# Performance work log

Measured on AMD Instinct MI355X. Metric: run time of the kernel, lower is better.

## Reference

```python
import jax, jax.numpy as jnp
import numpy as np

B, N, C, H = 64, 577, 768, 12
D = C // H
SCALE = D ** -0.5


def setup_inputs() -> dict:
    key = jax.random.key(0)
    ks = jax.random.split(key, 5)
    s = 0.02
    return {
        "x": jax.random.normal(ks[0], (B, N, C), dtype=jnp.float32),
        "qkv_w": jax.random.normal(ks[1], (3 * C, C), dtype=jnp.float32) * s,
        "qkv_b": jax.random.normal(ks[2], (3 * C,), dtype=jnp.float32) * s,
        "proj_w": jax.random.normal(ks[3], (C, C), dtype=jnp.float32) * s,
        "proj_b": jax.random.normal(ks[4], (C,), dtype=jnp.float32) * s,
    }


def reference(x, qkv_w, qkv_b, proj_w, proj_b):
    b, n, c = x.shape
    # Full QKV projection (as in the original module): [B,N,3C] -> [B,N,3,H,D]
    qkv = (x @ qkv_w.T + qkv_b).reshape(b, n, 3, H, D)
    qc = qkv[:, :1, 0]   # class-token query only: [B,1,H,D]
    k = qkv[:, :, 1]     # [B,N,H,D]
    v = qkv[:, :, 2]     # [B,N,H,D]
    # single-query attention scores per head: [B,H,N]
    attn = jnp.einsum("bohd,bnhd->bhn", qc, k) * SCALE
    attn = jax.nn.softmax(attn, axis=-1)
    # weighted sum of values -> [B,H,D] -> [B,1,C]
    cls = jnp.einsum("bhn,bnhd->bhd", attn, v).reshape(b, 1, c)
    cls = cls @ proj_w.T + proj_b
    return jnp.concatenate([cls, x[:, 1:]], axis=1)
```

## Files before the change

### kernel.cpp

```cpp
#include <hip/hip_runtime.h>

#define Bz 64
#define Nn 577
#define Cc 768
#define Hh 12
#define Dd 64
#define SCALE 0.125f

typedef __attribute__((ext_vector_type(8))) short short8;
typedef __attribute__((ext_vector_type(4))) float float4v;

__device__ __forceinline__ unsigned short bf16rne(float f) {
  unsigned u = __float_as_uint(f);
  u += 0x7FFFu + ((u >> 16) & 1u);
  return (unsigned short)(u >> 16);
}

__device__ __forceinline__ short8 cvt8(float4 a, float4 b) {
  short8 v;
  v[0] = (short)bf16rne(a.x); v[1] = (short)bf16rne(a.y);
  v[2] = (short)bf16rne(a.z); v[3] = (short)bf16rne(a.w);
  v[4] = (short)bf16rne(b.x); v[5] = (short)bf16rne(b.y);
  v[6] = (short)bf16rne(b.z); v[7] = (short)bf16rne(b.w);
  return v;
}


template <int MODE>
__global__ __launch_bounds__(256) void k_gemm64(const float* __restrict__ A,
                                                const float* __restrict__ W,
                                                const float* __restrict__ bias,
                                                float* __restrict__ out) {
  int tile = blockIdx.x;
  int jt = tile % 48, bt = tile / 48;
  int wave = threadIdx.x >> 6, lane = threadIdx.x & 63;
  int m = lane & 15, quad = lane >> 4;
  int brow = bt * 16 + m;
  int jrow = jt * 16 + m;
  size_t aoff;
  if (MODE == 0)      aoff = (size_t)brow * (Nn * Cc);
  else if (MODE == 1) aoff = (size_t)brow * (Hh * Cc) + (size_t)(jt >> 2) * Cc;
  else                aoff = (size_t)brow * Cc;
  size_t woff = (MODE == 1) ? (size_t)(2 * Cc + jrow) * Cc : (size_t)jrow * Cc;
  const float4* Ap = (const float4*)(A + aoff) + wave * 48 + quad * 2;
  const float4* Wp = (const float4*)(W + woff) + wave * 48 + quad * 2;
  float4v acc = {0.f, 0.f, 0.f, 0.f};
#pragma unroll
  for (int s = 0; s < 6; ++s) {
    float4 a0 = Ap[s * 8], a1 = Ap[s * 8 + 1];
    float4 w0 = Wp[s * 8], w1 = Wp[s * 8 + 1];
    acc = __builtin_amdgcn_mfma_f32_16x16x32_bf16(cvt8(a0, a1), cvt8(w0, w1),
                                                  acc, 0, 0, 0);
  }
  __shared__ float red[4][64][4];
#pragma unroll
  for (int reg = 0; reg < 4; ++reg) red[wave][lane][reg] = acc[reg];
  __syncthreads();
  if (wave == 0) {
#pragma unroll
    for (int reg = 0; reg < 4; ++reg) {
      float v = red[0][lane][reg] + red[1][lane][reg] +
                red[2][lane][reg] + red[3][lane][reg];
      int j = jt * 16 + m;
      int bb = bt * 16 + quad * 4 + reg;
      float bv = (MODE == 1) ? bias[2 * Cc + j] : bias[j];
      if (MODE == 2) out[(size_t)bb * (Nn * Cc) + j] = v + bv;
      else           out[(size_t)bb * Cc + j] = v + bv;
    }
  }
}

__global__ __launch_bounds__(256) void k_r(const float* __restrict__ qf,
                                           const float* __restrict__ qkv_w,
                                           unsigned short* __restrict__ rb) {
  int h = blockIdx.x % Hh, bg = blockIdx.x / Hh;
  int t = threadIdx.x;
  __shared__ float qs2[Dd][8];
  for (int idx = t; idx < 512; idx += 256) {
    int bb = idx >> 6, d = idx & 63;
    qs2[d][bb] = qf[(size_t)(bg * 8 + bb) * Cc + h * Dd + d];
  }
  __syncthreads();
  float acc[8][3];
#pragma unroll
  for (int bb = 0; bb < 8; ++bb)
#pragma unroll
    for (int i = 0; i < 3; ++i) acc[bb][i] = 0.f;
  const float* wk = qkv_w + (size_t)(Cc + h * Dd) * Cc;
  for (int d = 0; d < Dd; ++d) {
    float w0 = wk[(size_t)d * Cc + t];
    float w1 = wk[(size_t)d * Cc + t + 256];
    float w2 = wk[(size_t)d * Cc + t + 512];
    float4 qa = *(const float4*)&qs2[d][0];
    float4 qb = *(const float4*)&qs2[d][4];
    float qv[8] = {qa.x, qa.y, qa.z, qa.w, qb.x, qb.y, qb.z, qb.w};
#pragma unroll
    for (int bb = 0; bb < 8; ++bb) {
      acc[bb][0] += qv[bb] * w0;
      acc[bb][1] += qv[bb] * w1;
      acc[bb][2] += qv[bb] * w2;
    }
  }
#pragma unroll
  for (int bb = 0; bb < 8; ++bb) {
    size_t base = (size_t)(bg * 8 + bb) * 12288 + h * 8;
#pragma unroll
    for (int i = 0; i < 3; ++i) {
      int c = t + i * 256;
      int s = c >> 5, qq = (c >> 3) & 3, j = c & 7;
      rb[base + s * 512 + qq * 128 + j] = bf16rne(acc[bb][i] * SCALE);
    }
  }
}

__global__ __launch_bounds__(256) void k_logits(const float* __restrict__ x,
                                                const unsigned short* __restrict__ rb,
                                                float* __restrict__ logits) {
  int b = blockIdx.x / 10, tile = blockIdx.x % 10;
  int wave = threadIdx.x >> 6, lane = threadIdx.x & 63;
  int m = lane & 15, quad = lane >> 4;
  int n = tile * 64 + wave * 16 + m;
  int nc = n > 576 ? 576 : n;
  const short8* ag = (const short8*)(rb + (size_t)b * 12288);
  const float4* xg = (const float4*)(x + (size_t)b * Nn * Cc) +
                     (size_t)nc * 192 + quad * 2;
  float4v acc = {0.f, 0.f, 0.f, 0.f};
#pragma unroll 8
  for (int s = 0; s < 24; ++s) {
    short8 a = ag[s * 64 + quad * 16 + m];
    float4 f0 = xg[s * 8], f1 = xg[s * 8 + 1];
    acc = __builtin_amdgcn_mfma_f32_16x16x32_bf16(a, cvt8(f0, f1), acc, 0, 0, 0);
  }
  if (n < Nn) {
#pragma unroll
    for (int reg = 0; reg < 4; ++reg) {
      int hh = quad * 4 + reg;
      if (hh < Hh) logits[((size_t)b * Hh + hh) * Nn + n] = acc[reg];
    }
  }
}

__global__ __launch_bounds__(64) void k_softmax(const float* __restrict__ logits,
                                                float* __restrict__ attnT) {
  int bh = blockIdx.x;
  int b = bh / Hh, h = bh % Hh;
  const float* row = logits + (size_t)bh * Nn;
  int t = threadIdx.x;
  float vals[10];
  float m = -1e30f;
#pragma unroll
  for (int i = 0; i < 10; ++i) {
    int n = i * 64 + t;
    vals[i] = (n < Nn) ? row[n] : -1e30f;
    m = fmaxf(m, vals[i]);
  }
#pragma unroll
  for (int off = 32; off; off >>= 1) m = fmaxf(m, __shfl_down(m, off));
  m = __shfl(m, 0);
  float s = 0.f;
#pragma unroll
  for (int i = 0; i < 10; ++i) { vals[i] = __expf(vals[i] - m); s += vals[i]; }
#pragma unroll
  for (int off = 32; off; off >>= 1) s += __shfl_down(s, off);
  float inv = 1.f / __shfl(s, 0);
#pragma unroll
  for (int i = 0; i < 10; ++i) {
    int n = i * 64 + t;
    if (n < Nn) attnT[((size_t)b * Nn + n) * Hh + h] = vals[i] * inv;
  }
}

__global__ __launch_bounds__(256) void k_zero(float* __restrict__ y) {
  ((float4*)y)[blockIdx.x * 256 + threadIdx.x] = make_float4(0.f, 0.f, 0.f, 0.f);
}

#define YSEG 8
__global__ __launch_bounds__(192) void k_y(const float* __restrict__ x,
                                           const float* __restrict__ attnT,
                                           float* __restrict__ y) {
  int b = blockIdx.x / YSEG, seg = blockIdx.x % YSEG;
  int n0 = seg * Nn / YSEG, n1 = (seg + 1) * Nn / YSEG;
  int c4 = threadIdx.x;
  float4 acc[Hh];
#pragma unroll
  for (int h = 0; h < Hh; ++h) acc[h] = make_float4(0.f, 0.f, 0.f, 0.f);
  const float4* x4 = (const float4*)(x + (size_t)b * Nn * Cc);
  const float* at = attnT + (size_t)b * Nn * Hh;
#pragma unroll 8
  for (int n = n0; n < n1; ++n) {
    float4 xv = x4[(size_t)n * 192 + c4];
#pragma unroll
    for (int h = 0; h < Hh; ++h) {
      float a = at[n * Hh + h];
      acc[h].x += a * xv.x; acc[h].y += a * xv.y;
      acc[h].z += a * xv.z; acc[h].w += a * xv.w;
    }
  }
  float* yb = y + (size_t)b * Hh * Cc;
#pragma unroll
  for (int h = 0; h < Hh; ++h) {
    float* p = yb + h * Cc + c4 * 4;
    atomicAdd(p + 0, acc[h].x); atomicAdd(p + 1, acc[h].y);
    atomicAdd(p + 2, acc[h].z); atomicAdd(p + 3, acc[h].w);
  }
}

__global__ __launch_bounds__(256) void k_copy(const float* __restrict__ x,
                                              float* __restrict__ out) {
  int idx = blockIdx.x * 256 + threadIdx.x;
  const float4* xi = (const float4*)x;
  float4* oo = (float4*)out;
  for (int i = idx; i < 7077888; i += 262144) {
    int b = i / 110592;
    int r = i - b * 110592;
    size_t off = (size_t)b * 110784 + 192 + r;
    oo[off] = xi[off];
  }
}

extern "C" void kernel_launch(void* const* d_in, const int* in_sizes, int n_in,
                              void* d_out, int out_size, void* d_ws, size_t ws_size,
                              hipStream_t stream) {
  const float* x      = (const float*)d_in[0];
  const float* qkv_w  = (const float*)d_in[1];
  const float* qkv_b  = (const float*)d_in[2];
  const float* proj_w = (const float*)d_in[3];
  const float* proj_b = (const float*)d_in[4];
  float* out = (float*)d_out;
  float* ws = (float*)d_ws;

  unsigned short* rb = (unsigned short*)ws;
  float* qf     = ws + 393216;
  float* logits = ws + 442368;
  float* attnT  = ws + 885504;
  float* y      = ws + 1328640;
  float* cls    = ws + 1918464;

  k_zero<<<576, 256, 0, stream>>>(y);
  k_gemm64<0><<<192, 256, 0, stream>>>(x, qkv_w, qkv_b, qf);
  k_r<<<96, 256, 0, stream>>>(qf, qkv_w, rb);
  k_logits<<<Bz * 10, 256, 0, stream>>>(x, rb, logits);
  k_softmax<<<Bz * Hh, 64, 0, stream>>>(logits, attnT);
  k_y<<<Bz * YSEG, 192, 0, stream>>>(x, attnT, y);
  k_gemm64<1><<<192, 256, 0, stream>>>(y, qkv_w, qkv_b, cls);
  k_gemm64<2><<<192, 256, 0, stream>>>(cls, proj_w, proj_b, out);
  k_copy<<<1024, 256, 0, stream>>>(x, out);
}
```

Measured before the change: 356.8 us.

## Fuse x copy with bf16 pre-conversion, replace atomic y reduction with partial sums

Adds a prep kernel that reads x once, writes the passthrough rows of the output, and stores a bf16 copy of x that the logits kernel reads instead of fp32. The atomic y accumulation is replaced by a 576-thread kernel that reduces three row sub-ranges in shared memory and writes per-segment partials, which the V-projection GEMM sums while loading A. Fallback paths are kept for smaller workspaces. The bf16 copy adds a large extra write of x in exchange for halving the logits read and removing the separate copy and zero kernels.

```diff
diff --git a/kernel.cpp b/kernel.cpp
--- a/kernel.cpp
+++ b/kernel.cpp
@@ -6,6 +6,7 @@
 #define Hh 12
 #define Dd 64
 #define SCALE 0.125f
+#define YSEG 8
 
 typedef __attribute__((ext_vector_type(8))) short short8;
 typedef __attribute__((ext_vector_type(4))) float float4v;
@@ -25,8 +26,17 @@
   return v;
 }
 
-
-template <int MODE>
+__device__ __forceinline__ short8 cvt8v(float4v a, float4v b) {
+  short8 v;
+  v[0] = (short)bf16rne(a[0]); v[1] = (short)bf16rne(a[1]);
+  v[2] = (short)bf16rne(a[2]); v[3] = (short)bf16rne(a[3]);
+  v[4] = (short)bf16rne(b[0]); v[5] = (short)bf16rne(b[1]);
+  v[6] = (short)bf16rne(b[2]); v[7] = (short)bf16rne(b[3]);
+  return v;
+}
+
+
+template <int MODE, int SEGS>
 __global__ __launch_bounds__(256) void k_gemm64(const float* __restrict__ A,
                                                 const float* __restrict__ W,
                                                 const float* __restrict__ bias,
@@ -39,17 +49,28 @@
   int jrow = jt * 16 + m;
   size_t aoff;
   if (MODE == 0)      aoff = (size_t)brow * (Nn * Cc);
-  else if (MODE == 1) aoff = (size_t)brow * (Hh * Cc) + (size_t)(jt >> 2) * Cc;
+  else if (MODE == 1) aoff = (size_t)brow * (SEGS * Hh * Cc) + (size_t)(jt >> 2) * Cc;
   else                aoff = (size_t)brow * Cc;
   size_t woff = (MODE == 1) ? (size_t)(2 * Cc + jrow) * Cc : (size_t)jrow * Cc;
-  const float4* Ap = (const float4*)(A + aoff) + wave * 48 + quad * 2;
-  const float4* Wp = (const float4*)(W + woff) + wave * 48 + quad * 2;
+  const float4v* Ap = (const float4v*)(A + aoff) + wave * 48 + quad * 2;
+  const float4v* Wp = (const float4v*)(W + woff) + wave * 48 + quad * 2;
   float4v acc = {0.f, 0.f, 0.f, 0.f};
 #pragma unroll
   for (int s = 0; s < 6; ++s) {
-    float4 a0 = Ap[s * 8], a1 = Ap[s * 8 + 1];
-    float4 w0 = Wp[s * 8], w1 = Wp[s * 8 + 1];
-    acc = __builtin_amdgcn_mfma_f32_16x16x32_bf16(cvt8(a0, a1), cvt8(w0, w1),
+    float4v a0, a1;
+    if (MODE == 1 && SEGS > 1) {
+      a0 = (float4v){0.f, 0.f, 0.f, 0.f};
+      a1 = a0;
+#pragma unroll
+      for (int seg = 0; seg < SEGS; ++seg) {
+        a0 += Ap[seg * 2304 + s * 8];
+        a1 += Ap[seg * 2304 + s * 8 + 1];
+      }
+    } else {
+      a0 = Ap[s * 8]; a1 = Ap[s * 8 + 1];
+    }
+    float4v w0 = Wp[s * 8], w1 = Wp[s * 8 + 1];
+    acc = __builtin_amdgcn_mfma_f32_16x16x32_bf16(cvt8v(a0, a1), cvt8v(w0, w1),
                                                   acc, 0, 0, 0);
   }
   __shared__ float red[4][64][4];
@@ -113,7 +134,28 @@
   }
 }
 
+__global__ __launch_bounds__(256) void k_prep(const float* __restrict__ x,
+                                              float* __restrict__ out,
+                                              unsigned short* __restrict__ xbf) {
+  int i = blockIdx.x * 256 + threadIdx.x;
+  const float4v* xi = (const float4v*)x + (size_t)i * 4;
+  float4v a0 = xi[0], a1 = xi[1], a2 = xi[2], a3 = xi[3];
+  short8* xb = (short8*)xbf + (size_t)i * 2;
+  xb[0] = cvt8v(a0, a1);
+  xb[1] = cvt8v(a2, a3);
+  int r = i % (Nn * 48);
+  if (r >= 48) {
+    float4v* oo = (float4v*)out + (size_t)i * 4;
+    __builtin_nontemporal_store(a0, oo);
+    __builtin_nontemporal_store(a1, oo + 1);
+    __builtin_nontemporal_store(a2, oo + 2);
+    __builtin_nontemporal_store(a3, oo + 3);
+  }
+}
+
+template <int XBF>
 __global__ __launch_bounds__(256) void k_logits(const float* __restrict__ x,
+                                                const unsigned short* __restrict__ xbf,
                                                 const unsigned short* __restrict__ rb,
                                                 float* __restrict__ logits) {
   int b = blockIdx.x / 10, tile = blockIdx.x % 10;
@@ -122,14 +164,20 @@
   int n = tile * 64 + wave * 16 + m;
   int nc = n > 576 ? 576 : n;
   const short8* ag = (const short8*)(rb + (size_t)b * 12288);
-  const float4* xg = (const float4*)(x + (size_t)b * Nn * Cc) +
-                     (size_t)nc * 192 + quad * 2;
+  const short8* xg8 = (const short8*)(xbf + (size_t)b * Nn * Cc) + (size_t)nc * 96 + quad;
+  const float4* xg = (const float4*)(x + (size_t)b * Nn * Cc) + (size_t)nc * 192 + quad * 2;
   float4v acc = {0.f, 0.f, 0.f, 0.f};
 #pragma unroll 8
   for (int s = 0; s < 24; ++s) {
     short8 a = ag[s * 64 + quad * 16 + m];
-    float4 f0 = xg[s * 8], f1 = xg[s * 8 + 1];
-    acc = __builtin_amdgcn_mfma_f32_16x16x32_bf16(a, cvt8(f0, f1), acc, 0, 0, 0);
+    short8 bfrag;
+    if (XBF) {
+      bfrag = xg8[s * 4];
+    } else {
+      float4 f0 = xg[s * 8], f1 = xg[s * 8 + 1];
+      bfrag = cvt8(f0, f1);
+    }
+    acc = __builtin_amdgcn_mfma_f32_16x16x32_bf16(a, bfrag, acc, 0, 0, 0);
   }
   if (n < Nn) {
 #pragma unroll
@@ -170,14 +218,51 @@
   }
 }
 
+__global__ __launch_bounds__(576) void k_y3(const float* __restrict__ x,
+                                            const float* __restrict__ attnT,
+                                            float* __restrict__ ypart) {
+  int b = blockIdx.x / YSEG, seg = blockIdx.x % YSEG;
+  int c4 = threadIdx.x % 192;
+  int sub = threadIdx.x / 192;
+  int n0 = seg * Nn / YSEG, n1 = (seg + 1) * Nn / YSEG;
+  int len = n1 - n0;
+  int a0 = n0 + sub * len / 3, a1 = n0 + (sub + 1) * len / 3;
+  float4v acc[Hh];
+#pragma unroll
+  for (int h = 0; h < Hh; ++h) acc[h] = (float4v){0.f, 0.f, 0.f, 0.f};
+  const float4v* x4 = (const float4v*)(x + (size_t)b * Nn * Cc);
+  const float* at = attnT + (size_t)b * Nn * Hh;
+#pragma unroll 4
+  for (int n = a0; n < a1; ++n) {
+    float4v xv = x4[(size_t)n * 192 + c4];
+#pragma unroll
+    for (int h = 0; h < Hh; ++h) acc[h] += at[n * Hh + h] * xv;
+  }
+  __shared__ float4v red[192][Hh];
+  if (sub == 2) {
+#pragma unroll
+    for (int h = 0; h < Hh; ++h) red[c4][h] = acc[h];
+  }
+  __syncthreads();
+  if (sub == 1) {
+#pragma unroll
+    for (int h = 0; h < Hh; ++h) { acc[h] += red[c4][h]; red[c4][h] = acc[h]; }
+  }
+  __syncthreads();
+  if (sub == 0) {
+    float4v* yp = (float4v*)(ypart + ((size_t)(b * YSEG + seg)) * (Hh * Cc));
+#pragma unroll
+    for (int h = 0; h < Hh; ++h) yp[h * 192 + c4] = acc[h] + red[c4][h];
+  }
+}
+
 __global__ __launch_bounds__(256) void k_zero(float* __restrict__ y) {
   ((float4*)y)[blockIdx.x * 256 + threadIdx.x] = make_float4(0.f, 0.f, 0.f, 0.f);
 }
 
-#define YSEG 8
-__global__ __launch_bounds__(192) void k_y(const float* __restrict__ x,
-                                           const float* __restrict__ attnT,
-                                           float* __restrict__ y) {
+__global__ __launch_bounds__(192) void k_y_atomic(const float* __restrict__ x,
+                                                  const float* __restrict__ attnT,
+                                                  float* __restrict__ y) {
   int b = blockIdx.x / YSEG, seg = blockIdx.x % YSEG;
   int n0 = seg * Nn / YSEG, n1 = (seg + 1) * Nn / YSEG;
   int c4 = threadIdx.x;
@@ -233,16 +318,41 @@
   float* qf     = ws + 393216;
   float* logits = ws + 442368;
   float* attnT  = ws + 885504;
-  float* y      = ws + 1328640;
-  float* cls    = ws + 1918464;
-
-  k_zero<<<576, 256, 0, stream>>>(y);
-  k_gemm64<0><<<192, 256, 0, stream>>>(x, qkv_w, qkv_b, qf);
-  k_r<<<96, 256, 0, stream>>>(qf, qkv_w, rb);
-  k_logits<<<Bz * 10, 256, 0, stream>>>(x, rb, logits);
-  k_softmax<<<Bz * Hh, 64, 0, stream>>>(logits, attnT);
-  k_y<<<Bz * YSEG, 192, 0, stream>>>(x, attnT, y);
-  k_gemm64<1><<<192, 256, 0, stream>>>(y, qkv_w, qkv_b, cls);
-  k_gemm64<2><<<192, 256, 0, stream>>>(cls, proj_w, proj_b, out);
-  k_copy<<<1024, 256, 0, stream>>>(x, out);
-}
+  float* ypart  = ws + 1328640;
+  float* cls    = ws + 6047232;
+  unsigned short* xbf = (unsigned short*)(ws + 6096384);
+
+  const size_t NEED_XBF  = (size_t)(6096384 + 14180352) * 4;
+  const size_t NEED_PART = (size_t)6096384 * 4;
+
+  if (ws_size >= NEED_XBF) {
+    k_prep<<<6924, 256, 0, stream>>>(x, out, xbf);
+    k_gemm64<0, 1><<<192, 256, 0, stream>>>(x, qkv_w, qkv_b, qf);
+    k_r<<<96, 256, 0, stream>>>(qf, qkv_w, rb);
+    k_logits<1><<<Bz * 10, 256, 0, stream>>>(x, xbf, rb, logits);
+    k_softmax<<<Bz * Hh, 64, 0, stream>>>(logits, attnT);
+    k_y3<<<Bz * YSEG, 576, 0, stream>>>(x, attnT, ypart);
+    k_gemm64<1, YSEG><<<192, 256, 0, stream>>>(ypart, qkv_w, qkv_b, cls);
+    k_gemm64<2, 1><<<192, 256, 0, stream>>>(cls, proj_w, proj_b, out);
+  } else if (ws_size >= NEED_PART) {
+    k_gemm64<0, 1><<<192, 256, 0, stream>>>(x, qkv_w, qkv_b, qf);
+    k_r<<<96, 256, 0, stream>>>(qf, qkv_w, rb);
+    k_logits<0><<<Bz * 10, 256, 0, stream>>>(x, (const unsigned short*)x, rb, logits);
+    k_softmax<<<Bz * Hh, 64, 0, stream>>>(logits, attnT);
+    k_y3<<<Bz * YSEG, 576, 0, stream>>>(x, attnT, ypart);
+    k_gemm64<1, YSEG><<<192, 256, 0, stream>>>(ypart, qkv_w, qkv_b, cls);
+    k_gemm64<2, 1><<<192, 256, 0, stream>>>(cls, proj_w, proj_b, out);
+    k_copy<<<1024, 256, 0, stream>>>(x, out);
+  } else {
+    float* y     = ws + 1328640;
+    float* cls_c = ws + 1918464;
+    k_zero<<<576, 256, 0, stream>>>(y);
+    k_gemm64<0, 1><<<192, 256, 0, stream>>>(x, qkv_w, qkv_b, qf);
+    k_r<<<96, 256, 0, stream>>>(qf, qkv_w, rb);
+    k_logits<0><<<Bz * 10, 256, 0, stream>>>(x, (const unsigned short*)x, rb, logits);
+    k_softmax<<<Bz * Hh, 64, 0, stream>>>(logits, attnT);
+    k_y_atomic<<<Bz * YSEG, 192, 0, stream>>>(x, attnT, y);
+    k_gemm64<1, 1><<<192, 256, 0, stream>>>(y, qkv_w, qkv_b, cls_c);
+    k_gemm64<2, 1><<<192, 256, 0, stream>>>(cls_c, proj_w, proj_b, out);
+  }
+}
```

Measured after the change: 366.2 us. +2.6%, slower.
